# Kernel tuning notes

Hardware: AMD Instinct MI355X
Metric: run time of the kernel (lower is better)

## Reference

```python
import jax, jax.numpy as jnp
import numpy as np

NUM_LAYERS = 8
HIDDEN = 128
BATCH = 262144
SKIP_CONNECTION = True
BIAS_ENABLED = True


def setup_inputs() -> dict:
    key = jax.random.key(0)
    kx, kw, kb = jax.random.split(key, 3)
    x = jax.random.normal(kx, (BATCH, HIDDEN), dtype=jnp.float32)
    # scale weights ~ 1/sqrt(fan_in) so activations stay O(1) across 8 layers
    w = jax.random.normal(kw, (NUM_LAYERS, HIDDEN, HIDDEN), dtype=jnp.float32) * (1.0 / np.sqrt(HIDDEN))
    b = jax.random.normal(kb, (NUM_LAYERS, HIDDEN), dtype=jnp.float32) * 0.01
    return {"x": x, "w": w, "b": b}


def reference(x, w, b):
    # Fused elastic MLP, full-width (active_neurons == hidden for every layer).
    # Per the Triton forward kernel: every layer (including the last) applies
    # ReLU, and with skip_connection the input block is added AFTER the
    # activation for layers > 0.
    h = x
    for layer in range(NUM_LAYERS):
        h = jax.nn.relu(jnp.einsum('bi,ji->bj', h, w[layer]) + (b[layer] if BIAS_ENABLED else 0.0))
        if SKIP_CONNECTION and layer > 0:
            h = h + x  # input_dim == hidden, skip-add over full width
    return h
```

## Files before the change

### kernel.cpp

```cpp
#include <hip/hip_runtime.h>
#include <hip/hip_bf16.h>


typedef __bf16 bf16_t;
typedef __bf16 bf16x8 __attribute__((ext_vector_type(8)));
typedef float floatx4 __attribute__((ext_vector_type(4)));

#define HID 128
#define NLAYERS 8
#define TM 128
#define LDH 136

__global__ __launch_bounds__(256) void wconv_kernel(const float* __restrict__ w,
                                                    bf16_t* __restrict__ wb) {
    int i = blockIdx.x * 256 + threadIdx.x;
    wb[i] = (bf16_t)w[i];
}

__global__ __launch_bounds__(256, 2) void mlp_kernel(
    const float* __restrict__ x, const bf16_t* __restrict__ wb,
    const float* __restrict__ bias, float* __restrict__ out)
{
    __shared__ __align__(16) bf16_t hs[TM][LDH];
    __shared__ __align__(16) bf16_t wsh[HID][LDH];
    __shared__ float bs[HID];

    const int tid  = threadIdx.x;
    const int wave = tid >> 6;
    const int lane = tid & 63;
    const int c16  = lane & 15;
    const int quad = lane >> 4;
    const int m0 = (wave >> 1) * 64;
    const int n0 = (wave & 1) * 64;
    const long rowbase = (long)blockIdx.x * TM;

    float xr[4][4][4];
#pragma unroll
    for (int mi = 0; mi < 4; ++mi)
#pragma unroll
      for (int r = 0; r < 4; ++r) {
        const float* xrow = x + (rowbase + m0 + mi*16 + quad*4 + r) * HID;
#pragma unroll
        for (int ni = 0; ni < 4; ++ni)
          xr[mi][ni][r] = xrow[n0 + ni*16 + c16];
      }

#pragma unroll
    for (int mi = 0; mi < 4; ++mi)
#pragma unroll
      for (int ni = 0; ni < 4; ++ni)
#pragma unroll
        for (int r = 0; r < 4; ++r)
          hs[m0 + mi*16 + quad*4 + r][n0 + ni*16 + c16] = (bf16_t)xr[mi][ni][r];

    const bf16x8* wbv = (const bf16x8*)wb;
    bf16x8 wreg[8];
#pragma unroll
    for (int p = 0; p < 8; ++p) wreg[p] = wbv[p*256 + tid];
    float breg = (tid < HID) ? bias[tid] : 0.0f;

    for (int l = 0; l < NLAYERS; ++l) {
        __syncthreads();
#pragma unroll
        for (int p = 0; p < 8; ++p) {
            int f = p*256 + tid;
            *(bf16x8*)&wsh[f >> 4][(f & 15)*8] = wreg[p];
        }
        if (tid < HID) bs[tid] = breg;
        __syncthreads();

        if (l + 1 < NLAYERS) {
#pragma unroll
            for (int p = 0; p < 8; ++p) wreg[p] = wbv[(l+1)*2048 + p*256 + tid];
            if (tid < HID) breg = bias[(l+1)*HID + tid];
        }

        floatx4 acc[4][4];
#pragma unroll
        for (int mi = 0; mi < 4; ++mi)
#pragma unroll
          for (int ni = 0; ni < 4; ++ni)
            acc[mi][ni] = (floatx4)0.0f;

#pragma unroll
        for (int k = 0; k < 4; ++k) {
            const int kc = k*32 + quad*8;
            bf16x8 af[4], bfr[4];
#pragma unroll
            for (int mi = 0; mi < 4; ++mi)
                af[mi] = *(const bf16x8*)&hs[m0 + mi*16 + c16][kc];
#pragma unroll
            for (int ni = 0; ni < 4; ++ni)
                bfr[ni] = *(const bf16x8*)&wsh[n0 + ni*16 + c16][kc];
#pragma unroll
            for (int mi = 0; mi < 4; ++mi)
#pragma unroll
              for (int ni = 0; ni < 4; ++ni)
                acc[mi][ni] = __builtin_amdgcn_mfma_f32_16x16x32_bf16(
                                  af[mi], bfr[ni], acc[mi][ni], 0, 0, 0);
        }

        float bv[4];
#pragma unroll
        for (int ni = 0; ni < 4; ++ni) bv[ni] = bs[n0 + ni*16 + c16];

        if (l < NLAYERS - 1) {
            __syncthreads();
#pragma unroll
            for (int mi = 0; mi < 4; ++mi)
#pragma unroll
              for (int ni = 0; ni < 4; ++ni)
#pragma unroll
                for (int r = 0; r < 4; ++r) {
                    float v = acc[mi][ni][r] + bv[ni];
                    v = fmaxf(v, 0.0f);
                    if (l > 0) v += xr[mi][ni][r];
                    hs[m0 + mi*16 + quad*4 + r][n0 + ni*16 + c16] = (bf16_t)v;
                }
        } else {
#pragma unroll
            for (int mi = 0; mi < 4; ++mi)
#pragma unroll
              for (int r = 0; r < 4; ++r) {
                float* orow = out + (rowbase + m0 + mi*16 + quad*4 + r) * HID;
#pragma unroll
                for (int ni = 0; ni < 4; ++ni) {
                    float v = acc[mi][ni][r] + bv[ni];
                    v = fmaxf(v, 0.0f);
                    v += xr[mi][ni][r];
                    orow[n0 + ni*16 + c16] = v;
                }
              }
        }
    }
}

extern "C" void kernel_launch(void* const* d_in, const int* in_sizes, int n_in,
                              void* d_out, int out_size, void* d_ws, size_t ws_size,
                              hipStream_t stream) {
    const float* x = (const float*)d_in[0];
    const float* w = (const float*)d_in[1];
    const float* b = (const float*)d_in[2];
    float* out = (float*)d_out;
    bf16_t* wb = (bf16_t*)d_ws;

    wconv_kernel<<<NLAYERS*HID*HID/256, 256, 0, stream>>>(w, wb);

    const int nblocks = 262144 / TM;
    mlp_kernel<<<nblocks, 256, 0, stream>>>(x, wb, b, out);
}
```

Measured before the change: 294.2 us.

## Swap MFMA operands so accumulators hold contiguous feature runs for vector I/O

Computes the transposed product (weights as A, activations as B) so each lane's four accumulator values cover four consecutive output features of a single row. This allows float4 global loads of x, float4 output stores and 8-byte bf16x4 shared-memory writes in place of scalar accesses. The bias is folded into the accumulator initialisation, which removes its shared-memory buffer, and the per-layer barriers are rearranged. The weight conversion kernel is also vectorised four-wide. Risks include different LDS bank-conflict patterns and changed register pressure.

```diff
diff --git a/kernel.cpp b/kernel.cpp
--- a/kernel.cpp
+++ b/kernel.cpp
@@ -4,6 +4,7 @@
 
 typedef __bf16 bf16_t;
 typedef __bf16 bf16x8 __attribute__((ext_vector_type(8)));
+typedef __bf16 bf16x4 __attribute__((ext_vector_type(4)));
 typedef float floatx4 __attribute__((ext_vector_type(4)));
 
 #define HID 128
@@ -13,8 +14,10 @@
 
 __global__ __launch_bounds__(256) void wconv_kernel(const float* __restrict__ w,
                                                     bf16_t* __restrict__ wb) {
-    int i = blockIdx.x * 256 + threadIdx.x;
-    wb[i] = (bf16_t)w[i];
+    int i = (blockIdx.x * 256 + threadIdx.x) * 4;
+    floatx4 v = *(const floatx4*)&w[i];
+    bf16x4 o = { (bf16_t)v[0], (bf16_t)v[1], (bf16_t)v[2], (bf16_t)v[3] };
+    *(bf16x4*)&wb[i] = o;
 }
 
 __global__ __launch_bounds__(256, 2) void mlp_kernel(
@@ -23,7 +26,6 @@
 {
     __shared__ __align__(16) bf16_t hs[TM][LDH];
     __shared__ __align__(16) bf16_t wsh[HID][LDH];
-    __shared__ float bs[HID];
 
     const int tid  = threadIdx.x;
     const int wave = tid >> 6;
@@ -33,104 +35,110 @@
     const int m0 = (wave >> 1) * 64;
     const int n0 = (wave & 1) * 64;
     const long rowbase = (long)blockIdx.x * TM;
+    const int jb = m0 + quad * 4;
 
-    float xr[4][4][4];
+    floatx4 xr[4][4];
 #pragma unroll
-    for (int mi = 0; mi < 4; ++mi)
+    for (int ni = 0; ni < 4; ++ni) {
+        const float* xrow = x + (rowbase + n0 + ni*16 + c16) * HID;
 #pragma unroll
-      for (int r = 0; r < 4; ++r) {
-        const float* xrow = x + (rowbase + m0 + mi*16 + quad*4 + r) * HID;
+        for (int mi = 0; mi < 4; ++mi)
+            xr[mi][ni] = *(const floatx4*)&xrow[jb + mi*16];
+    }
 #pragma unroll
-        for (int ni = 0; ni < 4; ++ni)
-          xr[mi][ni][r] = xrow[n0 + ni*16 + c16];
-      }
-
+    for (int ni = 0; ni < 4; ++ni) {
+        bf16_t* hrow = &hs[n0 + ni*16 + c16][0];
 #pragma unroll
-    for (int mi = 0; mi < 4; ++mi)
-#pragma unroll
-      for (int ni = 0; ni < 4; ++ni)
-#pragma unroll
-        for (int r = 0; r < 4; ++r)
-          hs[m0 + mi*16 + quad*4 + r][n0 + ni*16 + c16] = (bf16_t)xr[mi][ni][r];
+        for (int mi = 0; mi < 4; ++mi) {
+            floatx4 v = xr[mi][ni];
+            bf16x4 o = { (bf16_t)v[0], (bf16_t)v[1], (bf16_t)v[2], (bf16_t)v[3] };
+            *(bf16x4*)&hrow[jb + mi*16] = o;
+        }
+    }
 
     const bf16x8* wbv = (const bf16x8*)wb;
     bf16x8 wreg[8];
 #pragma unroll
     for (int p = 0; p < 8; ++p) wreg[p] = wbv[p*256 + tid];
-    float breg = (tid < HID) ? bias[tid] : 0.0f;
+    floatx4 bnext[4];
+#pragma unroll
+    for (int mi = 0; mi < 4; ++mi) bnext[mi] = *(const floatx4*)&bias[jb + mi*16];
 
     for (int l = 0; l < NLAYERS; ++l) {
-        __syncthreads();
 #pragma unroll
         for (int p = 0; p < 8; ++p) {
             int f = p*256 + tid;
-            *(bf16x8*)&wsh[f >> 4][(f & 15)*8] = wreg[p];
+            *(bf16x8*)&wsh[f >> 4][(f & 15) * 8] = wreg[p];
         }
-        if (tid < HID) bs[tid] = breg;
         __syncthreads();
-
-        if (l + 1 < NLAYERS) {
-#pragma unroll
-            for (int p = 0; p < 8; ++p) wreg[p] = wbv[(l+1)*2048 + p*256 + tid];
-            if (tid < HID) breg = bias[(l+1)*HID + tid];
-        }
 
         floatx4 acc[4][4];
 #pragma unroll
         for (int mi = 0; mi < 4; ++mi)
 #pragma unroll
           for (int ni = 0; ni < 4; ++ni)
-            acc[mi][ni] = (floatx4)0.0f;
+            acc[mi][ni] = bnext[mi];
+
+        if (l + 1 < NLAYERS) {
+#pragma unroll
+            for (int p = 0; p < 8; ++p) wreg[p] = wbv[(l+1)*2048 + p*256 + tid];
+#pragma unroll
+            for (int mi = 0; mi < 4; ++mi)
+                bnext[mi] = *(const floatx4*)&bias[(l+1)*HID + jb + mi*16];
+        }
 
 #pragma unroll
         for (int k = 0; k < 4; ++k) {
             const int kc = k*32 + quad*8;
-            bf16x8 af[4], bfr[4];
+            bf16x8 af[4], bf[4];
 #pragma unroll
             for (int mi = 0; mi < 4; ++mi)
-                af[mi] = *(const bf16x8*)&hs[m0 + mi*16 + c16][kc];
+                af[mi] = *(const bf16x8*)&wsh[m0 + mi*16 + c16][kc];
 #pragma unroll
             for (int ni = 0; ni < 4; ++ni)
-                bfr[ni] = *(const bf16x8*)&wsh[n0 + ni*16 + c16][kc];
+                bf[ni] = *(const bf16x8*)&hs[n0 + ni*16 + c16][kc];
 #pragma unroll
             for (int mi = 0; mi < 4; ++mi)
 #pragma unroll
               for (int ni = 0; ni < 4; ++ni)
                 acc[mi][ni] = __builtin_amdgcn_mfma_f32_16x16x32_bf16(
-                                  af[mi], bfr[ni], acc[mi][ni], 0, 0, 0);
+                                  af[mi], bf[ni], acc[mi][ni], 0, 0, 0);
         }
-
-        float bv[4];
-#pragma unroll
-        for (int ni = 0; ni < 4; ++ni) bv[ni] = bs[n0 + ni*16 + c16];
+        __syncthreads();
 
         if (l < NLAYERS - 1) {
-            __syncthreads();
 #pragma unroll
-            for (int mi = 0; mi < 4; ++mi)
+            for (int ni = 0; ni < 4; ++ni) {
+                bf16_t* hrow = &hs[n0 + ni*16 + c16][0];
 #pragma unroll
-              for (int ni = 0; ni < 4; ++ni)
-#pragma unroll
-                for (int r = 0; r < 4; ++r) {
-                    float v = acc[mi][ni][r] + bv[ni];
-                    v = fmaxf(v, 0.0f);
-                    if (l > 0) v += xr[mi][ni][r];
-                    hs[m0 + mi*16 + quad*4 + r][n0 + ni*16 + c16] = (bf16_t)v;
+                for (int mi = 0; mi < 4; ++mi) {
+                    floatx4 v = acc[mi][ni];
+                    float s0 = fmaxf(v[0], 0.0f), s1 = fmaxf(v[1], 0.0f);
+                    float s2 = fmaxf(v[2], 0.0f), s3 = fmaxf(v[3], 0.0f);
+                    if (l > 0) {
+                        floatx4 xv = xr[mi][ni];
+                        s0 += xv[0]; s1 += xv[1]; s2 += xv[2]; s3 += xv[3];
+                    }
+                    bf16x4 o = { (bf16_t)s0, (bf16_t)s1, (bf16_t)s2, (bf16_t)s3 };
+                    *(bf16x4*)&hrow[jb + mi*16] = o;
                 }
+            }
         } else {
 #pragma unroll
-            for (int mi = 0; mi < 4; ++mi)
+            for (int ni = 0; ni < 4; ++ni) {
+                float* orow = out + (rowbase + n0 + ni*16 + c16) * HID;
 #pragma unroll
-              for (int r = 0; r < 4; ++r) {
-                float* orow = out + (rowbase + m0 + mi*16 + quad*4 + r) * HID;
-#pragma unroll
-                for (int ni = 0; ni < 4; ++ni) {
-                    float v = acc[mi][ni][r] + bv[ni];
-                    v = fmaxf(v, 0.0f);
-                    v += xr[mi][ni][r];
-                    orow[n0 + ni*16 + c16] = v;
+                for (int mi = 0; mi < 4; ++mi) {
+                    floatx4 v = acc[mi][ni];
+                    floatx4 xv = xr[mi][ni];
+                    floatx4 o;
+                    o[0] = fmaxf(v[0], 0.0f) + xv[0];
+                    o[1] = fmaxf(v[1], 0.0f) + xv[1];
+                    o[2] = fmaxf(v[2], 0.0f) + xv[2];
+                    o[3] = fmaxf(v[3], 0.0f) + xv[3];
+                    *(floatx4*)&orow[jb + mi*16] = o;
                 }
-              }
+            }
         }
     }
 }
@@ -144,7 +152,7 @@
     float* out = (float*)d_out;
     bf16_t* wb = (bf16_t*)d_ws;
 
-    wconv_kernel<<<NLAYERS*HID*HID/256, 256, 0, stream>>>(w, wb);
+    wconv_kernel<<<NLAYERS*HID*HID/(256*4), 256, 0, stream>>>(w, wb);
 
     const int nblocks = 262144 / TM;
     mlp_kernel<<<nblocks, 256, 0, stream>>>(x, wb, b, out);
```

Result: no change. 288.7 us (-1.9%).
